# Performance work log

Measured on AMD Instinct MI355X. Metric: run time of the kernel, lower is better.

## Reference

```python
import jax, jax.numpy as jnp
import numpy as np

DIM = 1024
N_HEADS = 16
WINDOW = 256
B, N = 16, 4096
ACC = 512
EPS = 1e-5


def setup_inputs() -> dict:
    key = jax.random.key(0)
    ks = jax.random.split(key, 16)
    D = DIM
    sc = 1.0 / np.sqrt(D)
    inp = {
        "x": jax.random.normal(ks[0], (B, N, D), dtype=jnp.float32),
        "state": jax.random.normal(ks[1], (B, D), dtype=jnp.float32),
        "acc_ctx": jax.random.normal(ks[2], (B, ACC, D), dtype=jnp.float32),
        "fix_pt": jax.random.randint(ks[3], (B,), 0, N, dtype=jnp.int32),
        # MultiheadAttention params (torch layout: in_proj_weight [3D, D])
        "in_proj_w": jax.random.normal(ks[4], (3 * D, D), dtype=jnp.float32) * sc,
        "in_proj_b": jnp.zeros((3 * D,), dtype=jnp.float32),
        "out_w": jax.random.normal(ks[5], (D, D), dtype=jnp.float32) * sc,
        "out_b": jnp.zeros((D,), dtype=jnp.float32),
        # LayerNorms
        "ln1_g": jnp.ones((D,), dtype=jnp.float32),
        "ln1_b": jnp.zeros((D,), dtype=jnp.float32),
        "ln2_g": jnp.ones((D,), dtype=jnp.float32),
        "ln2_b": jnp.zeros((D,), dtype=jnp.float32),
        # FFN: dim -> 4*dim -> dim (stored so that y = x @ w + b)
        "w1": jax.random.normal(ks[6], (D, 4 * D), dtype=jnp.float32) * sc,
        "b1": jnp.zeros((4 * D,), dtype=jnp.float32),
        "w2": jax.random.normal(ks[7], (4 * D, D), dtype=jnp.float32) * (1.0 / np.sqrt(4 * D)),
        "b2": jnp.zeros((D,), dtype=jnp.float32),
    }
    return inp


def _layer_norm(x, g, b):
    m = jnp.mean(x, axis=-1, keepdims=True)
    v = jnp.mean(jnp.square(x - m), axis=-1, keepdims=True)
    return (x - m) * jax.lax.rsqrt(v + EPS) * g + b


def _extract_windows(x, fix_pt):
    # Vectorized equivalent of the per-sample python loop. For even window_size
    # and N >= window_size the original logic reduces to a clamped start index.
    half = WINDOW // 2
    n = x.shape[1]
    start = jnp.clip(fix_pt - half, 0, n - WINDOW)  # [B]
    idx = start[:, None] + jnp.arange(WINDOW)       # [B, W]
    return jnp.take_along_axis(x, idx[:, :, None], axis=1)  # [B, W, D]


def _mha(xq, in_proj_w, in_proj_b, out_w, out_b):
    # torch nn.MultiheadAttention self-attention, batch_first
    Bq, L, D = xq.shape
    hd = D // N_HEADS
    qkv = xq @ in_proj_w.T + in_proj_b                     # [B, L, 3D]
    q, k, v = jnp.split(qkv, 3, axis=-1)
    def heads(t):
        return t.reshape(Bq, L, N_HEADS, hd).transpose(0, 2, 1, 3)  # [B,H,L,hd]
    q, k, v = heads(q), heads(k), heads(v)
    scores = jnp.einsum('bhqd,bhkd->bhqk', q, k) / np.sqrt(hd)
    attn = jax.nn.softmax(scores, axis=-1)
    o = jnp.einsum('bhqk,bhkd->bhqd', attn, v)             # [B,H,L,hd]
    o = o.transpose(0, 2, 1, 3).reshape(Bq, L, D)
    return o @ out_w.T + out_b


def reference(x, state, acc_ctx, in_proj_w, in_proj_b, out_w, out_b,
              ln1_g, ln1_b, ln2_g, ln2_b, w1, b1, w2, b2, fix_pt):
    window = _extract_windows(x, fix_pt)                   # [B, W, D]
    cls = state[:, None, :]                                # [B, 1, D]
    ctx = jnp.concatenate([cls, acc_ctx, window], axis=1)  # [B, 1+A+W, D]
    normed = _layer_norm(ctx, ln1_g, ln1_b)
    out = _mha(normed, in_proj_w, in_proj_b, out_w, out_b)
    ctx = ctx + out
    cls_out = ctx[:, 0]
    h = jax.nn.gelu(_layer_norm(cls_out, ln2_g, ln2_b) @ w1 + b1, approximate=False)
    cls_out = cls_out + h @ w2 + b2
    new_acc = jnp.concatenate([acc_ctx, window], axis=1)
    return cls_out, new_acc
```

## Files before the change

### kernel.cpp

```cpp
#include <hip/hip_runtime.h>
#include <hip/hip_bf16.h>
#include <math.h>

#define DIM 1024
#define NHEADS 16
#define HD 64
#define WIN 256
#define NB 16
#define NSEQ 4096
#define NACC 512
#define LCTX 769
#define MROWS 12304
#define MPAD2 12544
#define NKV 2048

typedef short bf16x8 __attribute__((ext_vector_type(8)));
typedef float f32x4 __attribute__((ext_vector_type(4)));

__device__ inline unsigned short f2b(float f) {
    union { float f; unsigned int u; } c; c.f = f;
    unsigned int u = c.u;
    u += 0x7FFFu + ((u >> 16) & 1u);
    return (unsigned short)(u >> 16);
}
__device__ inline float b2f(unsigned short h) {
    union { unsigned int u; float f; } c; c.u = ((unsigned int)h) << 16;
    return c.f;
}

__global__ __launch_bounds__(256) void build_ln_kernel(
    const float* __restrict__ x, const float* __restrict__ state,
    const float* __restrict__ acc_ctx, const int* __restrict__ fix_pt,
    const float* __restrict__ ln1_g, const float* __restrict__ ln1_b,
    const float* __restrict__ in_proj_w, unsigned short* __restrict__ Wb,
    unsigned short* __restrict__ normed, float* __restrict__ ctx0,
    float* __restrict__ newacc)
{
    int bid = blockIdx.x;
    int t = threadIdx.x;
    if (bid >= MPAD2) {
        int idx = (bid - MPAD2) * 256 + t;
        float4 v = ((const float4*)in_proj_w)[idx];
        ushort4 o;
        o.x = f2b(v.x); o.y = f2b(v.y); o.z = f2b(v.z); o.w = f2b(v.w);
        ((ushort4*)Wb)[idx] = o;
        return;
    }
    if (bid >= MROWS) {
        ushort4 z = make_ushort4(0, 0, 0, 0);
        ((ushort4*)(normed + (size_t)bid * DIM))[t] = z;
        return;
    }
    int b = bid / LCTX;
    int r = bid - b * LCTX;
    const float* src;
    if (r == 0) {
        src = state + (size_t)b * DIM;
    } else if (r <= NACC) {
        src = acc_ctx + ((size_t)b * NACC + (r - 1)) * DIM;
    } else {
        int fp = fix_pt[b];
        int start = fp - WIN / 2;
        if (start < 0) start = 0;
        if (start > NSEQ - WIN) start = NSEQ - WIN;
        src = x + ((size_t)b * NSEQ + start + (r - 1 - NACC)) * DIM;
    }
    float4 v = ((const float4*)src)[t];
    float s = v.x + v.y + v.z + v.w;
    float ss = v.x * v.x + v.y * v.y + v.z * v.z + v.w * v.w;
#pragma unroll
    for (int o = 32; o > 0; o >>= 1) { s += __shfl_down(s, o); ss += __shfl_down(ss, o); }
    __shared__ float rs[4], rss[4];
    int wid = t >> 6, lane = t & 63;
    if (lane == 0) { rs[wid] = s; rss[wid] = ss; }
    __syncthreads();
    float sum = rs[0] + rs[1] + rs[2] + rs[3];
    float sq  = rss[0] + rss[1] + rss[2] + rss[3];
    float mean = sum * (1.0f / DIM);
    float var = sq * (1.0f / DIM) - mean * mean;
    float rstd = rsqrtf(var + 1e-5f);
    float4 g  = ((const float4*)ln1_g)[t];
    float4 be = ((const float4*)ln1_b)[t];
    ushort4 nb;
    nb.x = f2b((v.x - mean) * rstd * g.x + be.x);
    nb.y = f2b((v.y - mean) * rstd * g.y + be.y);
    nb.z = f2b((v.z - mean) * rstd * g.z + be.z);
    nb.w = f2b((v.w - mean) * rstd * g.w + be.w);
    ((ushort4*)(normed + (size_t)bid * DIM))[t] = nb;
    if (r == 0) {
        ((float4*)(ctx0 + (size_t)b * DIM))[t] = v;
    } else {
        ((float4*)(newacc + ((size_t)b * (LCTX - 1) + (r - 1)) * DIM))[t] = v;
    }
}

__device__ inline void stage_half(const unsigned short* __restrict__ g,
                                  unsigned short* l, int t)
{
    {
        int r = t >> 3, c8 = (t & 7) ^ (r & 7);
        __builtin_amdgcn_global_load_lds(
            (const __attribute__((address_space(1))) void*)(g + (size_t)r * 1024 + c8 * 8),
            (__attribute__((address_space(3))) void*)(l + (size_t)t * 8), 16, 0, 0);
    }
    {
        int t2 = t + 512;
        int r = t2 >> 3, c8 = (t2 & 7) ^ (r & 7);
        __builtin_amdgcn_global_load_lds(
            (const __attribute__((address_space(1))) void*)(g + (size_t)r * 1024 + c8 * 8),
            (__attribute__((address_space(3))) void*)(l + (size_t)t2 * 8), 16, 0, 0);
    }
}

__device__ inline bf16x8 ldsw(const unsigned short* h, int r, int c8)
{
    int slot = r * 8 + (c8 ^ (r & 7));
    return *(const bf16x8*)(h + slot * 8);
}

__global__ __launch_bounds__(512, 2) void kv_gemm8_kernel(
    const unsigned short* __restrict__ A,
    const unsigned short* __restrict__ Bw,
    const float* __restrict__ bias,
    unsigned short* __restrict__ C)
{
    __shared__ unsigned short sh[2][2][2][128 * 64];
    const int mt = blockIdx.x >> 3, nt = blockIdx.x & 7;
    const int t = threadIdx.x;
    const int wid = t >> 6, lane = t & 63;
    const int wm = wid >> 2, wn = wid & 3;
    const int l15 = lane & 15, l16 = lane >> 4;
    const int rB = (wn & 1) * 64;
    const unsigned short* Abase = A + (size_t)mt * 256 * 1024;
    const unsigned short* Bbase = Bw + (size_t)nt * 256 * 1024;

    f32x4 acc[8][4] = {};
    bf16x8 a[4][2], b[4][2];

    stage_half(Abase,                   &sh[0][0][0][0], t);
    stage_half(Abase + 128 * 1024,      &sh[0][0][1][0], t);
    stage_half(Bbase,                   &sh[0][1][0][0], t);
    stage_half(Bbase + 128 * 1024,      &sh[0][1][1][0], t);
    stage_half(Bbase + 64,              &sh[1][1][0][0], t);
    stage_half(Bbase + 128 * 1024 + 64, &sh[1][1][1][0], t);
    asm volatile("s_waitcnt vmcnt(4)" ::: "memory");
    __builtin_amdgcn_s_barrier();

    auto ktile = [&](int T, bool stA, bool stB, bool steady) {
        const int d = T & 1;
        const unsigned short* AH = &sh[d][0][wm][0];
        const unsigned short* BH = &sh[d][1][wn >> 1][0];
        const int kA = (T + 1) * 64;
        const int kB = (T + 2) * 64;

#pragma unroll
        for (int i = 0; i < 4; ++i) {
            a[i][0] = ldsw(AH, i * 16 + l15, l16);
            a[i][1] = ldsw(AH, i * 16 + l15, 4 + l16);
        }
#pragma unroll
        for (int j = 0; j < 2; ++j) {
            b[j][0] = ldsw(BH, rB + j * 16 + l15, l16);
            b[j][1] = ldsw(BH, rB + j * 16 + l15, 4 + l16);
        }
        if (stA) stage_half(Abase + kA, &sh[d ^ 1][0][0][0], t);
        __builtin_amdgcn_sched_barrier(0);
        __builtin_amdgcn_s_barrier();
        asm volatile("s_waitcnt lgkmcnt(0)" ::: "memory");
        __builtin_amdgcn_sched_barrier(0);
        __builtin_amdgcn_s_setprio(1);
#pragma unroll
        for (int i = 0; i < 4; ++i)
#pragma unroll
            for (int j = 0; j < 2; ++j) {
                acc[i][j] = __builtin_amdgcn_mfma_f32_16x16x32_bf16(a[i][0], b[j][0], acc[i][j], 0, 0, 0);
                acc[i][j] = __builtin_amdgcn_mfma_f32_16x16x32_bf16(a[i][1], b[j][1], acc[i][j], 0, 0, 0);
            }
        __builtin_amdgcn_s_setprio(0);
        __builtin_amdgcn_sched_barrier(0);
        __builtin_amdgcn_s_barrier();

#pragma unroll
        for (int j = 2; j < 4; ++j) {
            b[j][0] = ldsw(BH, rB + j * 16 + l15, l16);
            b[j][1] = ldsw(BH, rB + j * 16 + l15, 4 + l16);
        }
        if (stA) stage_half(Abase + 128 * 1024 + kA, &sh[d ^ 1][0][1][0], t);
        __builtin_amdgcn_sched_barrier(0);
        __builtin_amdgcn_s_barrier();
        asm volatile("s_waitcnt lgkmcnt(0)" ::: "memory");
        __builtin_amdgcn_sched_barrier(0);
        __builtin_amdgcn_s_setprio(1);
#pragma unroll
        for (int i = 0; i < 4; ++i)
#pragma unroll
            for (int j = 2; j < 4; ++j) {
                acc[i][j] = __builtin_amdgcn_mfma_f32_16x16x32_bf16(a[i][0], b[j][0], acc[i][j], 0, 0, 0);
                acc[i][j] = __builtin_amdgcn_mfma_f32_16x16x32_bf16(a[i][1], b[j][1], acc[i][j], 0, 0, 0);
            }
        __builtin_amdgcn_s_setprio(0);
        __builtin_amdgcn_sched_barrier(0);
        __builtin_amdgcn_s_barrier();

#pragma unroll
        for (int i = 0; i < 4; ++i) {
            a[i][0] = ldsw(AH, 64 + i * 16 + l15, l16);
            a[i][1] = ldsw(AH, 64 + i * 16 + l15, 4 + l16);
        }
        if (stB) stage_half(Bbase + kB, &sh[d][1][0][0], t);
        __builtin_amdgcn_sched_barrier(0);
        __builtin_amdgcn_s_barrier();
        asm volatile("s_waitcnt lgkmcnt(0)" ::: "memory");
        __builtin_amdgcn_sched_barrier(0);
        __builtin_amdgcn_s_setprio(1);
#pragma unroll
        for (int i = 0; i < 4; ++i)
#pragma unroll
            for (int j = 0; j < 2; ++j) {
                acc[4 + i][j] = __builtin_amdgcn_mfma_f32_16x16x32_bf16(a[i][0], b[j][0], acc[4 + i][j], 0, 0, 0);
                acc[4 + i][j] = __builtin_amdgcn_mfma_f32_16x16x32_bf16(a[i][1], b[j][1], acc[4 + i][j], 0, 0, 0);
            }
        __builtin_amdgcn_s_setprio(0);
        __builtin_amdgcn_sched_barrier(0);
        __builtin_amdgcn_s_barrier();

        if (stB) stage_half(Bbase + 128 * 1024 + kB, &sh[d][1][1][0], t);
        __builtin_amdgcn_sched_barrier(0);
        __builtin_amdgcn_s_barrier();
        asm volatile("s_waitcnt lgkmcnt(0)" ::: "memory");
        __builtin_amdgcn_sched_barrier(0);
        __builtin_amdgcn_s_setprio(1);
#pragma unroll
        for (int i = 0; i < 4; ++i)
#pragma unroll
            for (int j = 2; j < 4; ++j) {
                acc[4 + i][j] = __builtin_amdgcn_mfma_f32_16x16x32_bf16(a[i][0], b[j][0], acc[4 + i][j], 0, 0, 0);
                acc[4 + i][j] = __builtin_amdgcn_mfma_f32_16x16x32_bf16(a[i][1], b[j][1], acc[4 + i][j], 0, 0, 0);
            }
        __builtin_amdgcn_s_setprio(0);
        if (steady) {
            asm volatile("s_waitcnt vmcnt(4)" ::: "memory");
        } else {
            asm volatile("s_waitcnt vmcnt(0)" ::: "memory");
        }
        __builtin_amdgcn_sched_barrier(0);
        __builtin_amdgcn_s_barrier();
    };

    for (int T = 0; T < 14; ++T) ktile(T, true, true, true);
    ktile(14, true, false, false);
    ktile(15, false, false, false);

#pragma unroll
    for (int i = 0; i < 8; ++i) {
        int gmb = mt * 256 + wm * 128 + i * 16 + l16 * 4;
#pragma unroll
        for (int j = 0; j < 4; ++j) {
            int gn = nt * 256 + wn * 64 + j * 16 + l15;
            float bs = bias[gn];
#pragma unroll
            for (int r = 0; r < 4; ++r) {
                int gm = gmb + r;
                if (gm < MROWS) C[(size_t)gm * NKV + gn] = f2b(acc[i][j][r] + bs);
            }
        }
    }
}

__global__ __launch_bounds__(512) void attn_kernel(
    const unsigned short* __restrict__ normed,
    const unsigned short* __restrict__ Wq, const float* __restrict__ bq,
    const unsigned short* __restrict__ kv, float* __restrict__ o_all)
{
    int b = blockIdx.x >> 4, h = blockIdx.x & 15;
    int t = threadIdx.x;
    int wave = t >> 6, lane = t & 63;
    __shared__ float qs[64];
    __shared__ float sc[LCTX];
    __shared__ float red1[8], red2[8];
    __shared__ float po[8][64];

    {
        const unsigned short* nr = normed + (size_t)(b * LCTX) * DIM;
        bf16x8 n0 = *(const bf16x8*)(nr + lane * 16);
        bf16x8 n1 = *(const bf16x8*)(nr + lane * 16 + 8);
#pragma unroll
        for (int jj = 0; jj < 8; ++jj) {
            int d = wave * 8 + jj;
            const unsigned short* wr = Wq + (size_t)(h * 64 + d) * DIM;
            bf16x8 w0 = *(const bf16x8*)(wr + lane * 16);
            bf16x8 w1 = *(const bf16x8*)(wr + lane * 16 + 8);
            float s = 0.f;
#pragma unroll
            for (int u = 0; u < 8; ++u)
                s += b2f((unsigned short)n0[u]) * b2f((unsigned short)w0[u]);
#pragma unroll
            for (int u = 0; u < 8; ++u)
                s += b2f((unsigned short)n1[u]) * b2f((unsigned short)w1[u]);
#pragma unroll
            for (int o = 32; o > 0; o >>= 1) s += __shfl_down(s, o);
            if (lane == 0) qs[d] = s + bq[h * 64 + d];
        }
    }
    __syncthreads();

    float lmax = -1e30f;
    for (int l = t; l < LCTX; l += 512) {
        const unsigned short* kr = kv + ((size_t)(b * LCTX + l)) * NKV + h * 64;
        const uint4* k4 = (const uint4*)kr;
        float s = 0.f;
#pragma unroll
        for (int c = 0; c < 8; ++c) {
            uint4 u = k4[c];
            s += qs[c * 8 + 0] * b2f((unsigned short)(u.x & 0xffffu));
            s += qs[c * 8 + 1] * b2f((unsigned short)(u.x >> 16));
            s += qs[c * 8 + 2] * b2f((unsigned short)(u.y & 0xffffu));
            s += qs[c * 8 + 3] * b2f((unsigned short)(u.y >> 16));
            s += qs[c * 8 + 4] * b2f((unsigned short)(u.z & 0xffffu));
            s += qs[c * 8 + 5] * b2f((unsigned short)(u.z >> 16));
            s += qs[c * 8 + 6] * b2f((unsigned short)(u.w & 0xffffu));
            s += qs[c * 8 + 7] * b2f((unsigned short)(u.w >> 16));
        }
        s *= 0.125f;
        sc[l] = s;
        lmax = fmaxf(lmax, s);
    }
#pragma unroll
    for (int o = 32; o > 0; o >>= 1) lmax = fmaxf(lmax, __shfl_down(lmax, o));
    if (lane == 0) red1[wave] = lmax;
    __syncthreads();
    float m = red1[0];
#pragma unroll
    for (int w8 = 1; w8 < 8; ++w8) m = fmaxf(m, red1[w8]);

    float lsum = 0.f;
    for (int l = t; l < LCTX; l += 512) {
        float p = __expf(sc[l] - m);
        sc[l] = p;
        lsum += p;
    }
#pragma unroll
    for (int o = 32; o > 0; o >>= 1) lsum += __shfl_down(lsum, o);
    if (lane == 0) red2[wave] = lsum;
    __syncthreads();
    float S = 0.f;
#pragma unroll
    for (int w8 = 0; w8 < 8; ++w8) S += red2[w8];

    int rg = lane >> 3;
    int dc = (lane & 7) * 8;
    float acc[8] = {};
    for (int it = 0; it < 13; ++it) {
        int row = it * 64 + wave * 8 + rg;
        if (row < LCTX) {
            const unsigned short* vr =
                kv + ((size_t)(b * LCTX + row)) * NKV + 1024 + h * 64 + dc;
            bf16x8 v = *(const bf16x8*)vr;
            float p = sc[row];
#pragma unroll
            for (int u = 0; u < 8; ++u) acc[u] += p * b2f((unsigned short)v[u]);
        }
    }
#pragma unroll
    for (int u = 0; u < 8; ++u) {
        acc[u] += __shfl_xor(acc[u], 8);
        acc[u] += __shfl_xor(acc[u], 16);
        acc[u] += __shfl_xor(acc[u], 32);
    }
    if (rg == 0) {
#pragma unroll
        for (int u = 0; u < 8; ++u) po[wave][dc + u] = acc[u];
    }
    __syncthreads();
    if (t < 64) {
        float o = 0.f;
#pragma unroll
        for (int w8 = 0; w8 < 8; ++w8) o += po[w8][t];
        o_all[b * 1024 + h * 64 + t] = o / S;
    }
}

__global__ __launch_bounds__(256) void out_proj_kernel(
    const float* __restrict__ o_all, const float* __restrict__ out_w,
    const float* __restrict__ out_b, const float* __restrict__ ctx0,
    float* __restrict__ cls_pre)
{
    int gw = blockIdx.x * 4 + (threadIdx.x >> 6);
    int lane = threadIdx.x & 63;
    int b = gw >> 10, i = gw & 1023;
    const float* orow = o_all + (size_t)b * 1024;
    const float* wrow = out_w + (size_t)i * 1024;
    float s = 0.f;
#pragma unroll
    for (int kk = 0; kk < 16; ++kk) {
        int k = kk * 64 + lane;
        s += orow[k] * wrow[k];
    }
#pragma unroll
    for (int o = 32; o > 0; o >>= 1) s += __shfl_down(s, o);
    if (lane == 0) cls_pre[gw] = ctx0[gw] + s + out_b[i];
}

__global__ __launch_bounds__(256) void ln2_kernel(
    const float* __restrict__ cls_pre, const float* __restrict__ g,
    const float* __restrict__ be, const float* __restrict__ b2,
    float* __restrict__ ln2o, float* __restrict__ outp)
{
    int b = blockIdx.x, t = threadIdx.x;
    float4 v = ((const float4*)(cls_pre + (size_t)b * DIM))[t];
    float s = v.x + v.y + v.z + v.w;
    float ss = v.x * v.x + v.y * v.y + v.z * v.z + v.w * v.w;
#pragma unroll
    for (int o = 32; o > 0; o >>= 1) { s += __shfl_down(s, o); ss += __shfl_down(ss, o); }
    __shared__ float rs[4], rss[4];
    int wid = t >> 6, lane = t & 63;
    if (lane == 0) { rs[wid] = s; rss[wid] = ss; }
    __syncthreads();
    float sum = rs[0] + rs[1] + rs[2] + rs[3];
    float sq  = rss[0] + rss[1] + rss[2] + rss[3];
    float mean = sum * (1.0f / DIM);
    float var = sq * (1.0f / DIM) - mean * mean;
    float rstd = rsqrtf(var + 1e-5f);
    float4 gv = ((const float4*)g)[t];
    float4 bv = ((const float4*)be)[t];
    float4 o;
    o.x = (v.x - mean) * rstd * gv.x + bv.x;
    o.y = (v.y - mean) * rstd * gv.y + bv.y;
    o.z = (v.z - mean) * rstd * gv.z + bv.z;
    o.w = (v.w - mean) * rstd * gv.w + bv.w;
    ((float4*)(ln2o + (size_t)b * DIM))[t] = o;
    float4 b2v = ((const float4*)b2)[t];
    float4 oi;
    oi.x = v.x + b2v.x; oi.y = v.y + b2v.y; oi.z = v.z + b2v.z; oi.w = v.w + b2v.w;
    ((float4*)(outp + (size_t)b * DIM))[t] = oi;
}

__global__ __launch_bounds__(256) void mlp1p_kernel(
    const float* __restrict__ ln2v, const float* __restrict__ w1,
    float* __restrict__ part)
{
    __shared__ float l2s[16][256];
    __shared__ float red[4][64][16];
    int jc = blockIdx.x, kq = blockIdx.y;
    int t = threadIdx.x;
#pragma unroll
    for (int b = 0; b < 16; ++b)
        l2s[b][t] = ln2v[(size_t)b * 1024 + kq * 256 + t];
    __syncthreads();
    int jl = t & 63, ks = t >> 6;
    int j = jc * 64 + jl;
    float acc[16] = {};
    for (int kk = 0; kk < 64; ++kk) {
        int kl = ks * 64 + kk;
        float wv = w1[(size_t)(kq * 256 + kl) * 4096 + j];
#pragma unroll
        for (int b = 0; b < 16; ++b) acc[b] += l2s[b][kl] * wv;
    }
#pragma unroll
    for (int b = 0; b < 16; ++b) red[ks][jl][b] = acc[b];
    __syncthreads();
    int jl2 = t & 63, bq = t >> 6;
#pragma unroll
    for (int bb = 0; bb < 4; ++bb) {
        int b = bq * 4 + bb;
        float s = red[0][jl2][b] + red[1][jl2][b] + red[2][jl2][b] + red[3][jl2][b];
        part[((size_t)kq * 16 + b) * 4096 + jc * 64 + jl2] = s;
    }
}

__global__ __launch_bounds__(256) void mlp2a_kernel(
    const float* __restrict__ part, const float* __restrict__ b1,
    const float* __restrict__ w2, float* __restrict__ outp)
{
    __shared__ float hseg[16][256];
    __shared__ float red[4][64][16];
    int ic = blockIdx.x, kq = blockIdx.y;
    int t = threadIdx.x;
    {
        int j = kq * 256 + t;
        float bb1 = b1[j];
#pragma unroll
        for (int b = 0; b < 16; ++b) {
            float s = part[((size_t)0 * 16 + b) * 4096 + j]
                    + part[((size_t)1 * 16 + b) * 4096 + j]
                    + part[((size_t)2 * 16 + b) * 4096 + j]
                    + part[((size_t)3 * 16 + b) * 4096 + j];
            s += bb1;
            hseg[b][t] = 0.5f * s * (1.0f + erff(s * 0.70710678118f));
        }
    }
    __syncthreads();
    int il = t & 63, ks = t >> 6;
    int i = ic * 64 + il;
    float acc[16] = {};
    for (int kk = 0; kk < 64; ++kk) {
        int kl = ks * 64 + kk;
        float wv = w2[(size_t)(kq * 256 + kl) * 1024 + i];
#pragma unroll
        for (int b = 0; b < 16; ++b) acc[b] += hseg[b][kl] * wv;
    }
#pragma unroll
    for (int b = 0; b < 16; ++b) red[ks][il][b] = acc[b];
    __syncthreads();
    int il2 = t & 63, bq = t >> 6;
#pragma unroll
    for (int bb = 0; bb < 4; ++bb) {
        int b = bq * 4 + bb;
        float s = red[0][il2][b] + red[1][il2][b] + red[2][il2][b] + red[3][il2][b];
        atomicAdd(&outp[(size_t)b * 1024 + ic * 64 + il2], s);
    }
}

extern "C" void kernel_launch(void* const* d_in, const int* in_sizes, int n_in,
                              void* d_out, int out_size, void* d_ws, size_t ws_size,
                              hipStream_t stream)
{
    const float* x        = (const float*)d_in[0];
    const float* state    = (const float*)d_in[1];
    const float* acc_ctx  = (const float*)d_in[2];
    const int*   fix_pt   = (const int*)d_in[3];
    const float* in_proj_w = (const float*)d_in[4];
    const float* in_proj_b = (const float*)d_in[5];
    const float* out_w    = (const float*)d_in[6];
    const float* out_b    = (const float*)d_in[7];
    const float* ln1_g    = (const float*)d_in[8];
    const float* ln1_b    = (const float*)d_in[9];
    const float* ln2_g    = (const float*)d_in[10];
    const float* ln2_b    = (const float*)d_in[11];
    const float* w1       = (const float*)d_in[12];
    const float* b1       = (const float*)d_in[13];
    const float* w2       = (const float*)d_in[14];
    const float* b2       = (const float*)d_in[15];
    float* outp = (float*)d_out;

    char* ws = (char*)d_ws;
    unsigned short* normed = (unsigned short*)ws; ws += (size_t)MPAD2 * DIM * 2;
    unsigned short* Wb     = (unsigned short*)ws; ws += (size_t)3072 * DIM * 2;
    unsigned short* kvb    = (unsigned short*)ws; ws += (size_t)MROWS * NKV * 2;
    float* ctx0    = (float*)ws; ws += (size_t)NB * DIM * 4;
    float* o_all   = (float*)ws; ws += (size_t)NB * DIM * 4;
    float* cls_pre = (float*)ws; ws += (size_t)NB * DIM * 4;
    float* ln2v    = (float*)ws; ws += (size_t)NB * DIM * 4;
    float* part    = (float*)ws; ws += (size_t)4 * 16 * 4096 * 4;

    float* newacc = outp + (size_t)NB * DIM;

    hipLaunchKernelGGL(build_ln_kernel, dim3(MPAD2 + 3072), dim3(256), 0, stream,
                       x, state, acc_ctx, fix_pt, ln1_g, ln1_b,
                       in_proj_w, Wb, normed, ctx0, newacc);
    hipLaunchKernelGGL(kv_gemm8_kernel, dim3(392), dim3(512), 0, stream,
                       normed, Wb + (size_t)1024 * DIM, in_proj_b + 1024, kvb);
    hipLaunchKernelGGL(attn_kernel, dim3(256), dim3(512), 0, stream,
                       normed, Wb, in_proj_b, kvb, o_all);
    hipLaunchKernelGGL(out_proj_kernel, dim3(4096), dim3(256), 0, stream,
                       o_all, out_w, out_b, ctx0, cls_pre);
    hipLaunchKernelGGL(ln2_kernel, dim3(16), dim3(256), 0, stream,
                       cls_pre, ln2_g, ln2_b, b2, ln2v, outp);
    hipLaunchKernelGGL(mlp1p_kernel, dim3(64, 4), dim3(256), 0, stream,
                       ln2v, w1, part);
    hipLaunchKernelGGL(mlp2a_kernel, dim3(16, 16), dim3(256), 0, stream,
                       part, b1, w2, outp);
}
```

Before: 165.2 us.

## Skip V projection by applying softmax weights to normed inputs then projecting

The V projection is no longer computed for all context rows. The attention kernel forms the softmax-weighted sum of the normed inputs per head and then multiplies that single vector by the V weight rows, using the identity sum p·(xW+b) = (sum p·x)W + b. This halves the big GEMM (K only, 4 N-tiles instead of 8) and the bf16 weight conversion. In exchange, each (batch, head) block now reads the full 769x1024 normed tile plus a 64x1024 fp32 weight slice, which repeats a lot of memory traffic across the 16 heads.

New measurement: 174.1 us. +5.4%, slower.

```diff
diff --git a/kernel.cpp b/kernel.cpp
--- a/kernel.cpp
+++ b/kernel.cpp
@@ -12,7 +12,6 @@
 #define LCTX 769
 #define MROWS 12304
 #define MPAD2 12544
-#define NKV 2048
 
 typedef short bf16x8 __attribute__((ext_vector_type(8)));
 typedef float f32x4 __attribute__((ext_vector_type(4)));
@@ -118,14 +117,14 @@
     return *(const bf16x8*)(h + slot * 8);
 }
 
-__global__ __launch_bounds__(512, 2) void kv_gemm8_kernel(
+__global__ __launch_bounds__(512, 2) void k_gemm8_kernel(
     const unsigned short* __restrict__ A,
     const unsigned short* __restrict__ Bw,
     const float* __restrict__ bias,
     unsigned short* __restrict__ C)
 {
     __shared__ unsigned short sh[2][2][2][128 * 64];
-    const int mt = blockIdx.x >> 3, nt = blockIdx.x & 7;
+    const int mt = blockIdx.x, nt = blockIdx.y;
     const int t = threadIdx.x;
     const int wid = t >> 6, lane = t & 63;
     const int wm = wid >> 2, wn = wid & 3;
@@ -261,24 +260,26 @@
 #pragma unroll
             for (int r = 0; r < 4; ++r) {
                 int gm = gmb + r;
-                if (gm < MROWS) C[(size_t)gm * NKV + gn] = f2b(acc[i][j][r] + bs);
+                if (gm < MROWS) C[(size_t)gm * 1024 + gn] = f2b(acc[i][j][r] + bs);
             }
         }
     }
 }
 
-__global__ __launch_bounds__(512) void attn_kernel(
+__global__ __launch_bounds__(512) void attn3_kernel(
     const unsigned short* __restrict__ normed,
-    const unsigned short* __restrict__ Wq, const float* __restrict__ bq,
-    const unsigned short* __restrict__ kv, float* __restrict__ o_all)
-{
-    int b = blockIdx.x >> 4, h = blockIdx.x & 15;
+    const unsigned short* __restrict__ Wqb, const float* __restrict__ in_proj_w,
+    const float* __restrict__ in_proj_b,
+    const unsigned short* __restrict__ kb, float* __restrict__ o_all)
+{
+    int b = blockIdx.x & 15, h = blockIdx.x >> 4;
     int t = threadIdx.x;
     int wave = t >> 6, lane = t & 63;
     __shared__ float qs[64];
     __shared__ float sc[LCTX];
     __shared__ float red1[8], red2[8];
-    __shared__ float po[8][64];
+    __shared__ float c4[4][1024];
+    __shared__ float cfin[1024];
 
     {
         const unsigned short* nr = normed + (size_t)(b * LCTX) * DIM;
@@ -287,7 +288,7 @@
 #pragma unroll
         for (int jj = 0; jj < 8; ++jj) {
             int d = wave * 8 + jj;
-            const unsigned short* wr = Wq + (size_t)(h * 64 + d) * DIM;
+            const unsigned short* wr = Wqb + (size_t)(h * 64 + d) * DIM;
             bf16x8 w0 = *(const bf16x8*)(wr + lane * 16);
             bf16x8 w1 = *(const bf16x8*)(wr + lane * 16 + 8);
             float s = 0.f;
@@ -299,14 +300,14 @@
                 s += b2f((unsigned short)n1[u]) * b2f((unsigned short)w1[u]);
 #pragma unroll
             for (int o = 32; o > 0; o >>= 1) s += __shfl_down(s, o);
-            if (lane == 0) qs[d] = s + bq[h * 64 + d];
+            if (lane == 0) qs[d] = s + in_proj_b[h * 64 + d];
         }
     }
     __syncthreads();
 
     float lmax = -1e30f;
     for (int l = t; l < LCTX; l += 512) {
-        const unsigned short* kr = kv + ((size_t)(b * LCTX + l)) * NKV + h * 64;
+        const unsigned short* kr = kb + ((size_t)(b * LCTX + l)) * 1024 + h * 64;
         const uint4* k4 = (const uint4*)kr;
         float s = 0.f;
 #pragma unroll
@@ -347,36 +348,38 @@
 #pragma unroll
     for (int w8 = 0; w8 < 8; ++w8) S += red2[w8];
 
-    int rg = lane >> 3;
-    int dc = (lane & 7) * 8;
-    float acc[8] = {};
-    for (int it = 0; it < 13; ++it) {
-        int row = it * 64 + wave * 8 + rg;
-        if (row < LCTX) {
-            const unsigned short* vr =
-                kv + ((size_t)(b * LCTX + row)) * NKV + 1024 + h * 64 + dc;
-            bf16x8 v = *(const bf16x8*)vr;
-            float p = sc[row];
-#pragma unroll
-            for (int u = 0; u < 8; ++u) acc[u] += p * b2f((unsigned short)v[u]);
-        }
-    }
-#pragma unroll
-    for (int u = 0; u < 8; ++u) {
-        acc[u] += __shfl_xor(acc[u], 8);
-        acc[u] += __shfl_xor(acc[u], 16);
-        acc[u] += __shfl_xor(acc[u], 32);
-    }
-    if (rg == 0) {
-#pragma unroll
-        for (int u = 0; u < 8; ++u) po[wave][dc + u] = acc[u];
-    }
-    __syncthreads();
-    if (t < 64) {
-        float o = 0.f;
-#pragma unroll
-        for (int w8 = 0; w8 < 8; ++w8) o += po[w8][t];
-        o_all[b * 1024 + h * 64 + t] = o / S;
+    const unsigned short* nb_ = normed + (size_t)(b * LCTX) * DIM;
+    int oc = t & 127;
+    int rg = t >> 7;
+    float ca[8] = {};
+    for (int l = rg; l < LCTX; l += 4) {
+        bf16x8 v = *(const bf16x8*)(nb_ + (size_t)l * DIM + oc * 8);
+        float p = sc[l];
+#pragma unroll
+        for (int u = 0; u < 8; ++u) ca[u] += p * b2f((unsigned short)v[u]);
+    }
+#pragma unroll
+    for (int u = 0; u < 8; ++u) c4[rg][oc * 8 + u] = ca[u];
+    __syncthreads();
+    for (int k = t; k < 1024; k += 512)
+        cfin[k] = c4[0][k] + c4[1][k] + c4[2][k] + c4[3][k];
+    __syncthreads();
+
+    float rS = 1.0f / S;
+#pragma unroll
+    for (int dd = 0; dd < 8; ++dd) {
+        int d = wave * 8 + dd;
+        const float* wr = in_proj_w + (size_t)(2048 + h * 64 + d) * DIM;
+        float s = 0.f;
+#pragma unroll
+        for (int kk = 0; kk < 16; ++kk) {
+            int k = kk * 64 + lane;
+            s += wr[k] * cfin[k];
+        }
+#pragma unroll
+        for (int o = 32; o > 0; o >>= 1) s += __shfl_down(s, o);
+        if (lane == 0)
+            o_all[b * 1024 + h * 64 + d] = s * rS + in_proj_b[2048 + h * 64 + d];
     }
 }
 
@@ -535,8 +538,8 @@
 
     char* ws = (char*)d_ws;
     unsigned short* normed = (unsigned short*)ws; ws += (size_t)MPAD2 * DIM * 2;
-    unsigned short* Wb     = (unsigned short*)ws; ws += (size_t)3072 * DIM * 2;
-    unsigned short* kvb    = (unsigned short*)ws; ws += (size_t)MROWS * NKV * 2;
+    unsigned short* Wb     = (unsigned short*)ws; ws += (size_t)2048 * DIM * 2;
+    unsigned short* kb     = (unsigned short*)ws; ws += (size_t)MROWS * 1024 * 2;
     float* ctx0    = (float*)ws; ws += (size_t)NB * DIM * 4;
     float* o_all   = (float*)ws; ws += (size_t)NB * DIM * 4;
     float* cls_pre = (float*)ws; ws += (size_t)NB * DIM * 4;
@@ -545,13 +548,13 @@
 
     float* newacc = outp + (size_t)NB * DIM;
 
-    hipLaunchKernelGGL(build_ln_kernel, dim3(MPAD2 + 3072), dim3(256), 0, stream,
+    hipLaunchKernelGGL(build_ln_kernel, dim3(MPAD2 + 2048), dim3(256), 0, stream,
                        x, state, acc_ctx, fix_pt, ln1_g, ln1_b,
                        in_proj_w, Wb, normed, ctx0, newacc);
-    hipLaunchKernelGGL(kv_gemm8_kernel, dim3(392), dim3(512), 0, stream,
-                       normed, Wb + (size_t)1024 * DIM, in_proj_b + 1024, kvb);
-    hipLaunchKernelGGL(attn_kernel, dim3(256), dim3(512), 0, stream,
-                       normed, Wb, in_proj_b, kvb, o_all);
+    hipLaunchKernelGGL(k_gemm8_kernel, dim3(49, 4), dim3(512), 0, stream,
+                       normed, Wb + (size_t)1024 * DIM, in_proj_b + 1024, kb);
+    hipLaunchKernelGGL(attn3_kernel, dim3(256), dim3(512), 0, stream,
+                       normed, Wb, in_proj_w, in_proj_b, kb, o_all);
     hipLaunchKernelGGL(out_proj_kernel, dim3(4096), dim3(256), 0, stream,
                        o_all, out_w, out_b, ctx0, cls_pre);
     hipLaunchKernelGGL(ln2_kernel, dim3(16), dim3(256), 0, stream,
```
